# Kernel optimization log

Hardware: AMD Instinct MI355X
Metric: run time of the kernel (lower is better)

The kernel has to match this reference:

```python
import jax, jax.numpy as jnp
import numpy as np

D_MODEL = 1024
NUM_HEADS = 16
HEAD_DIM = D_MODEL // NUM_HEADS


def setup_inputs() -> dict:
    key = jax.random.key(0)
    ks = jax.random.split(key, 5)
    B, S = 4, 2048
    scale = 0.02
    return {
        "x": jax.random.normal(ks[0], (B, S, D_MODEL), dtype=jnp.float32),
        "q_proj_weight": jax.random.normal(ks[1], (D_MODEL, D_MODEL), dtype=jnp.float32) * scale,
        "k_proj_weight": jax.random.normal(ks[2], (D_MODEL, D_MODEL), dtype=jnp.float32) * scale,
        "v_proj_weight": jax.random.normal(ks[3], (D_MODEL, D_MODEL), dtype=jnp.float32) * scale,
        "o_proj_weight": jax.random.normal(ks[4], (D_MODEL, D_MODEL), dtype=jnp.float32) * scale,
    }


def reference(x, q_proj_weight, k_proj_weight, v_proj_weight, o_proj_weight):
    B, S, _ = x.shape
    H, Dh = NUM_HEADS, HEAD_DIM

    def proj(w):  # [B,S,d_model] x [d_k,d_in] -> [B,H,S,Dh]
        p = jnp.einsum('bsd,kd->bsk', x, w)
        return p.reshape(B, S, H, Dh).transpose(0, 2, 1, 3)

    q = proj(q_proj_weight)
    k = proj(k_proj_weight)
    v = proj(v_proj_weight)

    scores = jnp.einsum('bhqd,bhkd->bhqk', q, k) / jnp.sqrt(jnp.asarray(Dh, dtype=x.dtype))
    causal = jnp.tril(jnp.ones((S, S), dtype=bool))  # [S,S]
    scores = jnp.where(causal, scores, -jnp.inf)
    attn = jax.nn.softmax(scores, axis=-1)
    out = jnp.einsum('bhqk,bhkd->bhqd', attn, v)  # [B,H,S,Dh]
    out = out.transpose(0, 2, 1, 3).reshape(B, S, D_MODEL)
    return jnp.einsum('bsv,mv->bsm', out, o_proj_weight)
```

## Files before the change

### kernel.cpp

```cpp
#include <hip/hip_runtime.h>
#include <cstdint>
#include <cstddef>

#define NH 16
#define DH 64
#define SEQ 2048
#define DM 1024

typedef __attribute__((ext_vector_type(8))) short short8;
typedef __attribute__((ext_vector_type(4))) float f32x4;

__device__ __forceinline__ unsigned short f2bf(float f) {
  unsigned u = __builtin_bit_cast(unsigned, f);
  u += 0x7fffu + ((u >> 16) & 1u);
  return (unsigned short)(u >> 16);
}

__device__ __forceinline__ void gld_lds16(const void* g, void* l) {
  __builtin_amdgcn_global_load_lds((const __attribute__((address_space(1))) void*)g,
                                   (__attribute__((address_space(3))) void*)l,
                                   16, 0, 0);
}

__global__ __launch_bounds__(256) void cast_all_kernel(const float* __restrict__ x,
                                                       const float* __restrict__ wq,
                                                       const float* __restrict__ wk,
                                                       const float* __restrict__ wv,
                                                       const float* __restrict__ wo,
                                                       unsigned short* __restrict__ xb,
                                                       unsigned short* __restrict__ wqkvb,
                                                       unsigned short* __restrict__ wob) {
  const int bid = blockIdx.x;
  const float* in;
  unsigned short* out;
  int i;
  if (bid < 8192) {
    in = x; out = xb; i = bid * 256 + threadIdx.x;
  } else {
    const int w = (bid - 8192) >> 10;
    i = ((bid - 8192) & 1023) * 256 + threadIdx.x;
    in = (w == 0) ? wq : (w == 1) ? wk : (w == 2) ? wv : wo;
    out = (w < 3) ? (wqkvb + (size_t)w * 1048576) : wob;
  }
  const float4 v = ((const float4*)in)[i];
  ushort4 o;
  o.x = f2bf(v.x); o.y = f2bf(v.y); o.z = f2bf(v.z); o.w = f2bf(v.w);
  ((ushort4*)out)[i] = o;
}

__global__ __launch_bounds__(512, 2) void gemm_qkv256(const unsigned short* __restrict__ A,
                                                      const unsigned short* __restrict__ W,
                                                      unsigned short* __restrict__ qb,
                                                      unsigned short* __restrict__ kb,
                                                      unsigned short* __restrict__ vtb) {
  extern __shared__ __align__(16) char sm[];

  const int t = threadIdx.x;
  const int lane = t & 63;
  const int wave = t >> 6;
  const int quad = lane >> 4;
  const int l16 = lane & 15;
  const int wr = wave >> 2;
  const int wc = wave & 3;

  const int bid = blockIdx.x;
  const int xcd = bid & 7;
  const int idx = bid >> 3;
  const int bm = (xcd * 4 + idx / 12) * 256;
  const int bn = (idx % 12) * 256;
  const int sel = bn >> 10;
  const int bnl = bn & 1023;

  f32x4 acc[8][4];
#pragma unroll
  for (int i = 0; i < 8; ++i)
#pragma unroll
    for (int j = 0; j < 4; ++j) acc[i][j] = {0.0f, 0.0f, 0.0f, 0.0f};

  const int r0s = t >> 3;
  const int g0 = (((t & 7) ^ (r0s & 7)) * 8);
  const unsigned short* aS0 = A + (size_t)(bm + r0s) * DM + g0;
  const unsigned short* aS1 = A + (size_t)(bm + 64 + r0s) * DM + g0;
  const unsigned short* bS0 = W + (size_t)(bn + r0s) * DM + g0;
  const unsigned short* bS1 = W + (size_t)(bn + 64 + r0s) * DM + g0;
  const int t16 = t * 16;

  const int aswz = (quad ^ (l16 & 7)) * 16;
  const int aRd0 = (wr * 128 + l16) * 128 + aswz;
  const int aRd1 = aRd0 ^ 64;
  const int bRd0 = 65536 + (wc * 64 + l16) * 128 + aswz;
  const int bRd1 = bRd0 ^ 64;

#define ST_A(U, TK, PAR)                                                                   \
  {                                                                                        \
    gld_lds16(aS0 + (size_t)(U) * 131072 + (TK) * 64, sm + (PAR) * 32768 + (U) * 16384 + t16); \
    gld_lds16(aS1 + (size_t)(U) * 131072 + (TK) * 64,                                      \
              sm + (PAR) * 32768 + (U) * 16384 + 8192 + t16);                              \
  }
#define ST_B(U, TK, PAR)                                                                   \
  {                                                                                        \
    gld_lds16(bS0 + (size_t)(U) * 131072 + (TK) * 64,                                      \
              sm + 65536 + (PAR) * 32768 + (U) * 16384 + t16);                             \
    gld_lds16(bS1 + (size_t)(U) * 131072 + (TK) * 64,                                      \
              sm + 65536 + (PAR) * 32768 + (U) * 16384 + 8192 + t16);                      \
  }

#define MM(AF, BF, IB, JB)                                                                 \
  _Pragma("unroll")                                                                        \
  for (int i = 0; i < 4; ++i)                                                              \
    _Pragma("unroll")                                                                      \
    for (int j = 0; j < 2; ++j) {                                                          \
      acc[(IB) + i][(JB) + j] = __builtin_amdgcn_mfma_f32_16x16x32_bf16(                   \
          AF[i][0], BF[j][0], acc[(IB) + i][(JB) + j], 0, 0, 0);                           \
      acc[(IB) + i][(JB) + j] = __builtin_amdgcn_mfma_f32_16x16x32_bf16(                   \
          AF[i][1], BF[j][1], acc[(IB) + i][(JB) + j], 0, 0, 0);                           \
    }

#define TILE(T, PAR, SB, SA, VM)                                                           \
  {                                                                                        \
    short8 af0[4][2], af1[4][2], bf0[2][2], bf1[2][2];                                     \
    _Pragma("unroll")                                                                      \
    for (int i = 0; i < 4; ++i) {                                                          \
      af0[i][0] = *(const short8*)(sm + (PAR) * 32768 + i * 2048 + aRd0);                  \
      af0[i][1] = *(const short8*)(sm + (PAR) * 32768 + i * 2048 + aRd1);                  \
    }                                                                                      \
    _Pragma("unroll")                                                                      \
    for (int j = 0; j < 2; ++j) {                                                          \
      bf0[j][0] = *(const short8*)(sm + (PAR) * 32768 + j * 2048 + bRd0);                  \
      bf0[j][1] = *(const short8*)(sm + (PAR) * 32768 + j * 2048 + bRd1);                  \
    }                                                                                      \
    if (SB) ST_B(0, (T) + 1, (PAR) ^ 1);                                                   \
    asm volatile("" ::: "memory");                                                         \
    __builtin_amdgcn_s_barrier();                                                          \
    asm volatile("s_waitcnt lgkmcnt(0)" ::: "memory");                                     \
    __builtin_amdgcn_s_setprio(1);                                                         \
    MM(af0, bf0, 0, 0);                                                                    \
    __builtin_amdgcn_s_setprio(0);                                                         \
    asm volatile("" ::: "memory");                                                         \
    __builtin_amdgcn_s_barrier();                                                          \
    _Pragma("unroll")                                                                      \
    for (int i = 0; i < 4; ++i) {                                                          \
      af1[i][0] = *(const short8*)(sm + (PAR) * 32768 + 8192 + i * 2048 + aRd0);           \
      af1[i][1] = *(const short8*)(sm + (PAR) * 32768 + 8192 + i * 2048 + aRd1);           \
    }                                                                                      \
    if (SB) ST_B(1, (T) + 1, (PAR) ^ 1);                                                   \
    asm volatile("" ::: "memory");                                                         \
    __builtin_amdgcn_s_barrier();                                                          \
    asm volatile("s_waitcnt lgkmcnt(0)" ::: "memory");                                     \
    __builtin_amdgcn_s_setprio(1);                                                         \
    MM(af1, bf0, 4, 0);                                                                    \
    __builtin_amdgcn_s_setprio(0);                                                         \
    asm volatile("" ::: "memory");                                                         \
    __builtin_amdgcn_s_barrier();                                                          \
    _Pragma("unroll")                                                                      \
    for (int j = 0; j < 2; ++j) {                                                          \
      bf1[j][0] = *(const short8*)(sm + (PAR) * 32768 + (2 + j) * 2048 + bRd0);            \
      bf1[j][1] = *(const short8*)(sm + (PAR) * 32768 + (2 + j) * 2048 + bRd1);            \
    }                                                                                      \
    if (SA) ST_A(0, (T) + 2, (PAR));                                                       \
    asm volatile("" ::: "memory");                                                         \
    __builtin_amdgcn_s_barrier();                                                          \
    asm volatile("s_waitcnt lgkmcnt(0)" ::: "memory");                                     \
    __builtin_amdgcn_s_setprio(1);                                                         \
    MM(af1, bf1, 4, 2);                                                                    \
    __builtin_amdgcn_s_setprio(0);                                                         \
    asm volatile("" ::: "memory");                                                         \
    __builtin_amdgcn_s_barrier();                                                          \
    if (SA) ST_A(1, (T) + 2, (PAR));                                                       \
    asm volatile("" ::: "memory");                                                         \
    __builtin_amdgcn_s_barrier();                                                          \
    __builtin_amdgcn_s_setprio(1);                                                         \
    MM(af0, bf1, 0, 2);                                                                    \
    __builtin_amdgcn_s_setprio(0);                                                         \
    if ((VM) == 4) asm volatile("s_waitcnt vmcnt(4)" ::: "memory");                        \
    else if ((VM) == 0) asm volatile("s_waitcnt vmcnt(0)" ::: "memory");                   \
    asm volatile("" ::: "memory");                                                         \
    __builtin_amdgcn_s_barrier();                                                          \
  }

  ST_A(0, 0, 0); ST_A(1, 0, 0);
  ST_B(0, 0, 0); ST_B(1, 0, 0);
  ST_A(0, 1, 1); ST_A(1, 1, 1);
  asm volatile("s_waitcnt vmcnt(4)" ::: "memory");
  __builtin_amdgcn_s_barrier();

#pragma unroll 1
  for (int tp = 0; tp < 7; ++tp) {
    const int T0 = tp * 2;
    TILE(T0, 0, 1, 1, 4)
    TILE(T0 + 1, 1, 1, 1, 4)
  }
  TILE(14, 0, 1, 0, 0)
  TILE(15, 1, 0, 0, -1)

#undef TILE
#undef MM
#undef ST_A
#undef ST_B

  if (sel == 2) {
    __syncthreads();
#pragma unroll
    for (int i = 0; i < 8; ++i) {
#pragma unroll
      for (int j = 0; j < 4; ++j) {
        const int n = wc * 64 + j * 16 + l16;
        const int nrow = n * 512;
        const int cswz = (n & 15) << 5;
        const int mb = wr * 128 + i * 16 + quad * 4;
#pragma unroll
        for (int rp = 0; rp < 2; ++rp) {
          const unsigned lo = f2bf(acc[i][j][rp * 2]);
          const unsigned hi = f2bf(acc[i][j][rp * 2 + 1]);
          const int m0 = mb + rp * 2;
          *(unsigned*)(sm + nrow + ((2 * m0) ^ cswz)) = lo | (hi << 16);
        }
      }
    }
    __syncthreads();
    const int mc = t & 31;
    const int nb0 = t >> 5;
    const int bb = bm >> 11;
    const int sbase = (bm & 2047) + mc * 8;
#pragma unroll
    for (int c = 0; c < 16; ++c) {
      const int n = nb0 + c * 16;
      const f32x4 v = *(const f32x4*)(sm + n * 512 + ((mc * 16) ^ ((n & 15) << 5)));
      const int gcol = bnl + n;
      const int h = gcol >> 6, d = gcol & 63;
      *(f32x4*)(vtb + ((size_t)((bb * NH + h) * DH + d)) * SEQ + sbase) = v;
    }
  } else {
#pragma unroll
    for (int i = 0; i < 8; ++i) {
#pragma unroll
      for (int j = 0; j < 4; ++j) {
#pragma unroll
        for (int r = 0; r < 4; ++r) {
          const int m = bm + wr * 128 + i * 16 + quad * 4 + r;
          const int n = bnl + wc * 64 + j * 16 + l16;
          const float v = acc[i][j][r];
          if (sel == 0) {
            qb[(size_t)m * DM + n] = f2bf(v * 0.125f);
          } else {
            kb[(size_t)m * DM + n] = f2bf(v);
          }
        }
      }
    }
  }
}

__global__ __launch_bounds__(256, 4) void gemm_o(const unsigned short* __restrict__ A,
                                                 const unsigned short* __restrict__ B,
                                                 float* __restrict__ C) {
  __shared__ __align__(16) unsigned short As[128 * 32];
  __shared__ __align__(16) unsigned short Bs[128 * 32];
  const int t = threadIdx.x;
  const int lane = t & 63;
  const int wave = t >> 6;
  const int quad = lane >> 4;
  const int l16 = lane & 15;
  const int wm = (wave >> 1) * 64;
  const int wn = (wave & 1) * 64;

  const int lid = blockIdx.x + 8 * blockIdx.y;
  const int xcd = lid & 7;
  const int idx = lid >> 3;
  const int bm = (xcd * 8 + idx / 8) * 128;
  const int bn = (idx % 8) * 128;

  f32x4 acc[4][4];
#pragma unroll
  for (int i = 0; i < 4; ++i)
#pragma unroll
    for (int j = 0; j < 4; ++j) acc[i][j] = {0.0f, 0.0f, 0.0f, 0.0f};

  const int srow = t >> 2;
  const int sc = (t & 3) ^ ((srow >> 1) & 3);
  const unsigned short* Ag1 = A + (size_t)(bm + srow) * DM + sc * 8;
  const unsigned short* Ag2 = A + (size_t)(bm + srow + 64) * DM + sc * 8;
  const unsigned short* Bg1 = B + (size_t)(bn + srow) * DM + sc * 8;
  const unsigned short* Bg2 = B + (size_t)(bn + srow + 64) * DM + sc * 8;
  const int swz = (l16 >> 1) & 3;

  for (int k0 = 0; k0 < DM; k0 += 32) {
    __syncthreads();
    gld_lds16(Ag1 + k0, As + t * 8);
    gld_lds16(Ag2 + k0, As + t * 8 + 2048);
    gld_lds16(Bg1 + k0, Bs + t * 8);
    gld_lds16(Bg2 + k0, Bs + t * 8 + 2048);
    __syncthreads();
    short8 af[4], bfr[4];
#pragma unroll
    for (int i = 0; i < 4; ++i)
      af[i] = *(const short8*)(As + (wm + i * 16 + l16) * 32 + ((quad ^ swz) * 8));
#pragma unroll
    for (int j = 0; j < 4; ++j)
      bfr[j] = *(const short8*)(Bs + (wn + j * 16 + l16) * 32 + ((quad ^ swz) * 8));
#pragma unroll
    for (int i = 0; i < 4; ++i)
#pragma unroll
      for (int j = 0; j < 4; ++j)
        acc[i][j] = __builtin_amdgcn_mfma_f32_16x16x32_bf16(af[i], bfr[j], acc[i][j], 0, 0, 0);
  }

#pragma unroll
  for (int i = 0; i < 4; ++i)
#pragma unroll
    for (int j = 0; j < 4; ++j)
#pragma unroll
      for (int r = 0; r < 4; ++r) {
        const int m = bm + wm + i * 16 + quad * 4 + r;
        const int n = bn + wn + j * 16 + l16;
        C[(size_t)m * DM + n] = acc[i][j][r];
      }
}

__global__ __launch_bounds__(512) void attn_kernel(const unsigned short* __restrict__ Q,
                                                   const unsigned short* __restrict__ K,
                                                   const unsigned short* __restrict__ Vt,
                                                   unsigned short* __restrict__ O) {
  extern __shared__ __align__(16) char asmem[];
  const int t = threadIdx.x;
  const int lane = t & 63;
  const int wave = t >> 6;
  const int quad = lane >> 4;
  const int l16 = lane & 15;
  const int h = blockIdx.y;
  const int b = blockIdx.z;

  const int ksr1 = t >> 3;
  const int ksr2 = (t + 512) >> 3;
  const int koff1 = (b * SEQ + ksr1) * DM + h * 64 + (((t & 7) ^ (ksr1 & 7)) * 8);
  const int koff2 = (b * SEQ + ksr2) * DM + h * 64 + (((t & 7) ^ (ksr2 & 7)) * 8);
  const int vsr1 = t >> 4;
  const int vsr2 = (t + 512) >> 4;
  const int voff1 = ((b * NH + h) * DH + vsr1) * SEQ + (((t & 15) ^ (vsr1 & 15)) * 8);
  const int voff2 = ((b * NH + h) * DH + vsr2) * SEQ + (((t & 15) ^ (vsr2 & 15)) * 8);
  unsigned short* Pw = (unsigned short*)(asmem + 65536) + wave * (16 * 136);
  const int swz = l16 & 7;

#define ATT_STAGE(KB, BUF)                                              \
  {                                                                     \
    char* kd = asmem + (BUF) * 16384;                                   \
    char* vd = asmem + 32768 + (BUF) * 16384;                           \
    gld_lds16(K + koff1 + (size_t)(KB) * DM, kd + t * 16);              \
    gld_lds16(K + koff2 + (size_t)(KB) * DM, kd + (t + 512) * 16);      \
    gld_lds16(Vt + voff1 + (KB), vd + t * 16);                          \
    gld_lds16(Vt + voff2 + (KB), vd + (t + 512) * 16);                  \
  }

#pragma unroll 1
  for (int pass = 0; pass < 2; ++pass) {
    const int qt = (pass == 0) ? (int)blockIdx.x : 15 - (int)blockIdx.x;
    const int qtile = qt * 128;
    const int row_lo = qtile + wave * 16;

    const unsigned short* Qrow =
        Q + ((size_t)(b * SEQ + row_lo + l16)) * DM + h * 64;
    const short8 qf0 = *(const short8*)(Qrow + quad * 8);
    const short8 qf1 = *(const short8*)(Qrow + 32 + quad * 8);

    f32x4 o_acc[4];
#pragma unroll
    for (int nb = 0; nb < 4; ++nb) o_acc[nb] = {0.0f, 0.0f, 0.0f, 0.0f};
    float l_r[4] = {0.0f, 0.0f, 0.0f, 0.0f};

    const int ktiles = qt + 1;
    ATT_STAGE(0, 0);
#pragma unroll 1
    for (int kt = 0; kt < ktiles; ++kt) {
      const int kbase = kt * 128;
      if (kt + 1 < ktiles) {
        ATT_STAGE((kt + 1) * 128, (kt + 1) & 1);
        asm volatile("s_waitcnt vmcnt(4)" ::: "memory");
      } else {
        asm volatile("s_waitcnt vmcnt(0)" ::: "memory");
      }
      __builtin_amdgcn_s_barrier();
      asm volatile("" ::: "memory");
      const unsigned short* Ksb = (const unsigned short*)(asmem + (kt & 1) * 16384);
      const unsigned short* Vsb = (const unsigned short*)(asmem + 32768 + (kt & 1) * 16384);

      f32x4 s_acc[8];
#pragma unroll
      for (int nb = 0; nb < 8; ++nb) {
        s_acc[nb] = {0.0f, 0.0f, 0.0f, 0.0f};
        const short8 kf0 = *(const short8*)(Ksb + (nb * 16 + l16) * 64 + ((quad ^ swz) * 8));
        const short8 kf1 = *(const short8*)(Ksb + (nb * 16 + l16) * 64 + (((4 | quad) ^ swz) * 8));
        s_acc[nb] = __builtin_amdgcn_mfma_f32_16x16x32_bf16(qf0, kf0, s_acc[nb], 0, 0, 0);
        s_acc[nb] = __builtin_amdgcn_mfma_f32_16x16x32_bf16(qf1, kf1, s_acc[nb], 0, 0, 0);
      }

      const bool need_mask = (kbase + 127 > row_lo);
#pragma unroll
      for (int r = 0; r < 4; ++r) {
        const int qr = row_lo + quad * 4 + r;
#pragma unroll
        for (int nb = 0; nb < 8; ++nb) {
          float p = __expf(s_acc[nb][r]);
          if (need_mask) p = ((kbase + nb * 16 + l16) <= qr) ? p : 0.0f;
          l_r[r] += p;
          const unsigned u = __builtin_bit_cast(unsigned, p);
          Pw[(quad * 4 + r) * 136 + nb * 16 + l16] =
              (unsigned short)((u + 0x8000u) >> 16);
        }
      }

#pragma unroll
      for (int kk = 0; kk < 4; ++kk) {
        const short8 pf = *(const short8*)(Pw + l16 * 136 + kk * 32 + quad * 8);
#pragma unroll
        for (int nb = 0; nb < 4; ++nb) {
          const short8 vf = *(const short8*)(Vsb + (nb * 16 + l16) * 128 +
                                             (((kk * 4 + quad) ^ l16) * 8));
          o_acc[nb] = __builtin_amdgcn_mfma_f32_16x16x32_bf16(pf, vf, o_acc[nb], 0, 0, 0);
        }
      }

      asm volatile("" ::: "memory");
      __builtin_amdgcn_s_barrier();
    }

#pragma unroll
    for (int r = 0; r < 4; ++r) {
      float ls = l_r[r];
      ls += __shfl_xor(ls, 1);
      ls += __shfl_xor(ls, 2);
      ls += __shfl_xor(ls, 4);
      ls += __shfl_xor(ls, 8);
      const float inv_l = 1.0f / ls;
      const int qr = row_lo + quad * 4 + r;
#pragma unroll
      for (int nb = 0; nb < 4; ++nb)
        O[((size_t)(b * SEQ + qr)) * DM + h * 64 + nb * 16 + l16] =
            f2bf(o_acc[nb][r] * inv_l);
    }
  }
#undef ATT_STAGE
}

extern "C" void kernel_launch(void* const* d_in, const int* in_sizes, int n_in,
                              void* d_out, int out_size, void* d_ws, size_t ws_size,
                              hipStream_t stream) {
  const float* x  = (const float*)d_in[0];
  const float* wq = (const float*)d_in[1];
  const float* wk = (const float*)d_in[2];
  const float* wv = (const float*)d_in[3];
  const float* wo = (const float*)d_in[4];

  char* ws = (char*)d_ws;
  unsigned short* xb    = (unsigned short*)(ws);
  unsigned short* wqkvb = (unsigned short*)(ws + 16777216);
  unsigned short* wob   = (unsigned short*)(ws + 23068672);
  unsigned short* qb    = (unsigned short*)(ws + 25165824);
  unsigned short* kb    = (unsigned short*)(ws + 41943040);
  unsigned short* vtb   = (unsigned short*)(ws + 58720256);
  unsigned short* aob   = (unsigned short*)(ws + 75497472);

  static bool s_attr_done = false;
  if (!s_attr_done) {
    hipFuncSetAttribute(reinterpret_cast<const void*>(gemm_qkv256),
                        hipFuncAttributeMaxDynamicSharedMemorySize, 131072);
    hipFuncSetAttribute(reinterpret_cast<const void*>(attn_kernel),
                        hipFuncAttributeMaxDynamicSharedMemorySize, 100352);
    s_attr_done = true;
  }

  cast_all_kernel<<<12288, 256, 0, stream>>>(x, wq, wk, wv, wo, xb, wqkvb, wob);

  gemm_qkv256<<<dim3(384), dim3(512), 131072, stream>>>(xb, wqkvb, qb, kb, vtb);

  attn_kernel<<<dim3(8, NH, 4), 512, 100352, stream>>>(qb, kb, vtb, aob);

  gemm_o<<<dim3(8, 64), 256, 0, stream>>>(aob, wob, (float*)d_out);
}
```

Baseline: 258.8 us.

## Process two 128-row query tiles per attention block to reuse K/V tiles

Each attention workgroup now handles a 256-row query span as two 128-row sub-tiles, so every K/V tile staged into LDS feeds two sets of score and PV MFMAs. Causal pairing still balances work across the two passes, and the grid is flattened to 256 blocks with a remapped (b,h,j) index that spreads heads across XCD-interleaved block IDs. The aim is to halve the K/V global-to-LDS traffic per unit of compute. In exchange, register pressure rises from doubled accumulators, LDS use grows, and the grid shrinks from 512 to 256 blocks, which may leave compute units underused.

```diff
diff --git a/kernel.cpp b/kernel.cpp
--- a/kernel.cpp
+++ b/kernel.cpp
@@ -327,8 +327,13 @@
   const int wave = t >> 6;
   const int quad = lane >> 4;
   const int l16 = lane & 15;
-  const int h = blockIdx.y;
-  const int b = blockIdx.z;
+
+  const int lid = blockIdx.x;
+  const int g = (lid & 7) * 32 + (lid >> 3);
+  const int j = g & 3;
+  const int bh = g >> 2;
+  const int h = bh & 15;
+  const int b = bh >> 4;
 
   const int ksr1 = t >> 3;
   const int ksr2 = (t + 512) >> 3;
@@ -338,7 +343,8 @@
   const int vsr2 = (t + 512) >> 4;
   const int voff1 = ((b * NH + h) * DH + vsr1) * SEQ + (((t & 15) ^ (vsr1 & 15)) * 8);
   const int voff2 = ((b * NH + h) * DH + vsr2) * SEQ + (((t & 15) ^ (vsr2 & 15)) * 8);
-  unsigned short* Pw = (unsigned short*)(asmem + 65536) + wave * (16 * 136);
+  unsigned short* Pw0 = (unsigned short*)(asmem + 65536) + wave * (2 * 16 * 136);
+  unsigned short* Pw1 = Pw0 + 16 * 136;
   const int swz = l16 & 7;
 
 #define ATT_STAGE(KB, BUF)                                              \
@@ -353,21 +359,25 @@
 
 #pragma unroll 1
   for (int pass = 0; pass < 2; ++pass) {
-    const int qt = (pass == 0) ? (int)blockIdx.x : 15 - (int)blockIdx.x;
-    const int qtile = qt * 128;
-    const int row_lo = qtile + wave * 16;
-
-    const unsigned short* Qrow =
-        Q + ((size_t)(b * SEQ + row_lo + l16)) * DM + h * 64;
-    const short8 qf0 = *(const short8*)(Qrow + quad * 8);
-    const short8 qf1 = *(const short8*)(Qrow + 32 + quad * 8);
-
-    f32x4 o_acc[4];
-#pragma unroll
-    for (int nb = 0; nb < 4; ++nb) o_acc[nb] = {0.0f, 0.0f, 0.0f, 0.0f};
-    float l_r[4] = {0.0f, 0.0f, 0.0f, 0.0f};
-
-    const int ktiles = qt + 1;
+    const int js = (pass == 0) ? j : 7 - j;
+    const int qs = js * 256;
+    const int rl0 = qs + wave * 16;
+    const int rl1 = rl0 + 128;
+
+    const unsigned short* Qr0 = Q + ((size_t)(b * SEQ + rl0 + l16)) * DM + h * 64;
+    const unsigned short* Qr1 = Q + ((size_t)(b * SEQ + rl1 + l16)) * DM + h * 64;
+    const short8 qf00 = *(const short8*)(Qr0 + quad * 8);
+    const short8 qf01 = *(const short8*)(Qr0 + 32 + quad * 8);
+    const short8 qf10 = *(const short8*)(Qr1 + quad * 8);
+    const short8 qf11 = *(const short8*)(Qr1 + 32 + quad * 8);
+
+    f32x4 o0[4], o1[4];
+#pragma unroll
+    for (int nb = 0; nb < 4; ++nb) { o0[nb] = {0.0f, 0.0f, 0.0f, 0.0f}; o1[nb] = {0.0f, 0.0f, 0.0f, 0.0f}; }
+    float l0[4] = {0.0f, 0.0f, 0.0f, 0.0f};
+    float l1[4] = {0.0f, 0.0f, 0.0f, 0.0f};
+
+    const int ktiles = 2 * js + 2;
     ATT_STAGE(0, 0);
 #pragma unroll 1
     for (int kt = 0; kt < ktiles; ++kt) {
@@ -383,39 +393,77 @@
       const unsigned short* Ksb = (const unsigned short*)(asmem + (kt & 1) * 16384);
       const unsigned short* Vsb = (const unsigned short*)(asmem + 32768 + (kt & 1) * 16384);
 
-      f32x4 s_acc[8];
+      const bool act0 = (kbase < qs + 128);
+
+      f32x4 s0[8], s1[8];
 #pragma unroll
       for (int nb = 0; nb < 8; ++nb) {
-        s_acc[nb] = {0.0f, 0.0f, 0.0f, 0.0f};
         const short8 kf0 = *(const short8*)(Ksb + (nb * 16 + l16) * 64 + ((quad ^ swz) * 8));
         const short8 kf1 = *(const short8*)(Ksb + (nb * 16 + l16) * 64 + (((4 | quad) ^ swz) * 8));
-        s_acc[nb] = __builtin_amdgcn_mfma_f32_16x16x32_bf16(qf0, kf0, s_acc[nb], 0, 0, 0);
-        s_acc[nb] = __builtin_amdgcn_mfma_f32_16x16x32_bf16(qf1, kf1, s_acc[nb], 0, 0, 0);
-      }
-
-      const bool need_mask = (kbase + 127 > row_lo);
-#pragma unroll
-      for (int r = 0; r < 4; ++r) {
-        const int qr = row_lo + quad * 4 + r;
-#pragma unroll
-        for (int nb = 0; nb < 8; ++nb) {
-          float p = __expf(s_acc[nb][r]);
-          if (need_mask) p = ((kbase + nb * 16 + l16) <= qr) ? p : 0.0f;
-          l_r[r] += p;
-          const unsigned u = __builtin_bit_cast(unsigned, p);
-          Pw[(quad * 4 + r) * 136 + nb * 16 + l16] =
-              (unsigned short)((u + 0x8000u) >> 16);
-        }
-      }
-
-#pragma unroll
-      for (int kk = 0; kk < 4; ++kk) {
-        const short8 pf = *(const short8*)(Pw + l16 * 136 + kk * 32 + quad * 8);
-#pragma unroll
-        for (int nb = 0; nb < 4; ++nb) {
-          const short8 vf = *(const short8*)(Vsb + (nb * 16 + l16) * 128 +
-                                             (((kk * 4 + quad) ^ l16) * 8));
-          o_acc[nb] = __builtin_amdgcn_mfma_f32_16x16x32_bf16(pf, vf, o_acc[nb], 0, 0, 0);
+        s1[nb] = {0.0f, 0.0f, 0.0f, 0.0f};
+        s1[nb] = __builtin_amdgcn_mfma_f32_16x16x32_bf16(qf10, kf0, s1[nb], 0, 0, 0);
+        s1[nb] = __builtin_amdgcn_mfma_f32_16x16x32_bf16(qf11, kf1, s1[nb], 0, 0, 0);
+        if (act0) {
+          s0[nb] = {0.0f, 0.0f, 0.0f, 0.0f};
+          s0[nb] = __builtin_amdgcn_mfma_f32_16x16x32_bf16(qf00, kf0, s0[nb], 0, 0, 0);
+          s0[nb] = __builtin_amdgcn_mfma_f32_16x16x32_bf16(qf01, kf1, s0[nb], 0, 0, 0);
+        }
+      }
+
+      if (act0) {
+        const bool nm0 = (kbase + 127 > rl0);
+#pragma unroll
+        for (int r = 0; r < 4; ++r) {
+          const int qr = rl0 + quad * 4 + r;
+#pragma unroll
+          for (int nb = 0; nb < 8; ++nb) {
+            float p = __expf(s0[nb][r]);
+            if (nm0) p = ((kbase + nb * 16 + l16) <= qr) ? p : 0.0f;
+            l0[r] += p;
+            const unsigned u = __builtin_bit_cast(unsigned, p);
+            Pw0[(quad * 4 + r) * 136 + nb * 16 + l16] = (unsigned short)((u + 0x8000u) >> 16);
+          }
+        }
+      }
+      {
+        const bool nm1 = (kbase + 127 > rl1);
+#pragma unroll
+        for (int r = 0; r < 4; ++r) {
+          const int qr = rl1 + quad * 4 + r;
+#pragma unroll
+          for (int nb = 0; nb < 8; ++nb) {
+            float p = __expf(s1[nb][r]);
+            if (nm1) p = ((kbase + nb * 16 + l16) <= qr) ? p : 0.0f;
+            l1[r] += p;
+            const unsigned u = __builtin_bit_cast(unsigned, p);
+            Pw1[(quad * 4 + r) * 136 + nb * 16 + l16] = (unsigned short)((u + 0x8000u) >> 16);
+          }
+        }
+      }
+
+      if (act0) {
+#pragma unroll
+        for (int kk = 0; kk < 4; ++kk) {
+          const short8 pf0 = *(const short8*)(Pw0 + l16 * 136 + kk * 32 + quad * 8);
+          const short8 pf1 = *(const short8*)(Pw1 + l16 * 136 + kk * 32 + quad * 8);
+#pragma unroll
+          for (int nb = 0; nb < 4; ++nb) {
+            const short8 vf = *(const short8*)(Vsb + (nb * 16 + l16) * 128 +
+                                               (((kk * 4 + quad) ^ l16) * 8));
+            o0[nb] = __builtin_amdgcn_mfma_f32_16x16x32_bf16(pf0, vf, o0[nb], 0, 0, 0);
+            o1[nb] = __builtin_amdgcn_mfma_f32_16x16x32_bf16(pf1, vf, o1[nb], 0, 0, 0);
+          }
+        }
+      } else {
+#pragma unroll
+        for (int kk = 0; kk < 4; ++kk) {
+          const short8 pf1 = *(const short8*)(Pw1 + l16 * 136 + kk * 32 + quad * 8);
+#pragma unroll
+          for (int nb = 0; nb < 4; ++nb) {
+            const short8 vf = *(const short8*)(Vsb + (nb * 16 + l16) * 128 +
+                                               (((kk * 4 + quad) ^ l16) * 8));
+            o1[nb] = __builtin_amdgcn_mfma_f32_16x16x32_bf16(pf1, vf, o1[nb], 0, 0, 0);
+          }
         }
       }
 
@@ -425,17 +473,31 @@
 
 #pragma unroll
     for (int r = 0; r < 4; ++r) {
-      float ls = l_r[r];
+      float ls = l0[r];
       ls += __shfl_xor(ls, 1);
       ls += __shfl_xor(ls, 2);
       ls += __shfl_xor(ls, 4);
       ls += __shfl_xor(ls, 8);
       const float inv_l = 1.0f / ls;
-      const int qr = row_lo + quad * 4 + r;
+      const int qr = rl0 + quad * 4 + r;
 #pragma unroll
       for (int nb = 0; nb < 4; ++nb)
         O[((size_t)(b * SEQ + qr)) * DM + h * 64 + nb * 16 + l16] =
-            f2bf(o_acc[nb][r] * inv_l);
+            f2bf(o0[nb][r] * inv_l);
+    }
+#pragma unroll
+    for (int r = 0; r < 4; ++r) {
+      float ls = l1[r];
+      ls += __shfl_xor(ls, 1);
+      ls += __shfl_xor(ls, 2);
+      ls += __shfl_xor(ls, 4);
+      ls += __shfl_xor(ls, 8);
+      const float inv_l = 1.0f / ls;
+      const int qr = rl1 + quad * 4 + r;
+#pragma unroll
+      for (int nb = 0; nb < 4; ++nb)
+        O[((size_t)(b * SEQ + qr)) * DM + h * 64 + nb * 16 + l16] =
+            f2bf(o1[nb][r] * inv_l);
     }
   }
 #undef ATT_STAGE
@@ -464,7 +526,7 @@
     hipFuncSetAttribute(reinterpret_cast<const void*>(gemm_qkv256),
                         hipFuncAttributeMaxDynamicSharedMemorySize, 131072);
     hipFuncSetAttribute(reinterpret_cast<const void*>(attn_kernel),
-                        hipFuncAttributeMaxDynamicSharedMemorySize, 100352);
+                        hipFuncAttributeMaxDynamicSharedMemorySize, 135168);
     s_attr_done = true;
   }
 
@@ -472,7 +534,7 @@
 
   gemm_qkv256<<<dim3(384), dim3(512), 131072, stream>>>(xb, wqkvb, qb, kb, vtb);
 
-  attn_kernel<<<dim3(8, NH, 4), 512, 100352, stream>>>(qb, kb, vtb, aob);
+  attn_kernel<<<dim3(256), dim3(512), 135168, stream>>>(qb, kb, vtb, aob);
 
   gemm_o<<<dim3(8, 64), 256, 0, stream>>>(aob, wob, (float*)d_out);
 }
```

Result: faster. 246.1 us (-4.9%).
